# Performance work log

Measured on AMD Instinct MI355X. Metric: run time of the kernel, lower is better.

## Reference

```python
import jax, jax.numpy as jnp
import numpy as np

MAXLEN = 30
VOCAB_SIZE = 20000
THOUGHT = 1200
WORD = 620
BATCH = 130  # decoder uses B-2 = 128 sequences


def setup_inputs() -> dict:
    key = jax.random.key(0)
    ks = jax.random.split(key, 8)
    s_ih = 1.0 / np.sqrt(WORD)
    return {
        "thoughts": jax.random.normal(ks[0], (BATCH, THOUGHT), dtype=jnp.float32),
        "embed_table": jax.random.normal(ks[1], (VOCAB_SIZE, WORD), dtype=jnp.float32),
        "W_ih": jax.random.uniform(ks[2], (4 * WORD, 2 * THOUGHT + WORD), jnp.float32, -s_ih, s_ih),
        "W_hh": jax.random.uniform(ks[3], (4 * WORD, WORD), jnp.float32, -s_ih, s_ih),
        "b_ih": jax.random.uniform(ks[4], (4 * WORD,), jnp.float32, -s_ih, s_ih),
        "b_hh": jax.random.uniform(ks[5], (4 * WORD,), jnp.float32, -s_ih, s_ih),
        "Ww": jax.random.uniform(ks[6], (VOCAB_SIZE, WORD), jnp.float32, -s_ih, s_ih),
        "bw": jax.random.uniform(ks[7], (VOCAB_SIZE,), jnp.float32, -s_ih, s_ih),
    }


def reference(thoughts, embed_table, W_ih, W_hh, b_ih, b_hh, Ww, bw):
    # context: concat(thoughts_prev, thoughts_next) -> [B-2, 2*THOUGHT]
    ctx = jnp.concatenate([thoughts[:-2], thoughts[2:]], axis=1)
    n = ctx.shape[0]
    h0 = jnp.zeros((n, WORD), dtype=thoughts.dtype)  # (h,c) reset to 0 each step

    def step(last_word, _):
        x = jnp.concatenate([ctx, last_word], axis=1)  # [n, 3020]
        # LSTM cell with zero initial state (original discards state each step)
        gates = x @ W_ih.T + b_ih + h0 @ W_hh.T + b_hh  # [n, 4*WORD]
        i, f, g, o = jnp.split(gates, 4, axis=1)
        c = jax.nn.sigmoid(i) * jnp.tanh(g)  # f-gate irrelevant, c_prev = 0
        h = jax.nn.sigmoid(o) * jnp.tanh(c)  # [n, WORD]
        logits = h @ Ww.T + bw               # [n, VOCAB]
        idx = jnp.argmax(logits, axis=1)
        new_last = embed_table[idx]          # greedy-decoded word embedding
        return new_last, h

    _, hs = jax.lax.scan(step, h0, None, length=MAXLEN)  # [MAXLEN, n, WORD]
    pred = jnp.einsum("tnw,vw->tnv", hs, Ww) + bw        # [MAXLEN, n, VOCAB]
    return jnp.transpose(pred, (1, 0, 2))                 # [n, MAXLEN, VOCAB]
```

## Files before the change

### kernel.cpp

```cpp
#include <hip/hip_runtime.h>
#include <math.h>

#define VOCAB 20000
#define WORD 620
#define NSEQ 128
#define TMAX 30
#define CTXK 2400
#define XK 3020
#define NBLK 256

typedef unsigned long long u64;
typedef __attribute__((ext_vector_type(8))) short short8;
typedef __attribute__((ext_vector_type(4))) float f32x4;

__device__ __forceinline__ unsigned ford(float f) {
    unsigned b = __float_as_uint(f);
    return (b & 0x80000000u) ? ~b : (b | 0x80000000u);
}
__device__ __forceinline__ unsigned short bf16rne(float x) {
    unsigned u = __float_as_uint(x);
    return (unsigned short)((u + 0x7fffu + ((u >> 16) & 1u)) >> 16);
}
__device__ __forceinline__ float bf16tof(unsigned short h) {
    return __uint_as_float(((unsigned)h) << 16);
}
__device__ __forceinline__ short8 ld8(const unsigned short* p) {
    return *(const short8*)p;
}
#define MFMA(a, b, c) __builtin_amdgcn_mfma_f32_16x16x32_bf16((a), (b), (c), 0, 0, 0)
#define VMW(N) asm volatile("s_waitcnt vmcnt(" #N ")" ::: "memory")
#define AL64(p) __hip_atomic_load((p), __ATOMIC_RELAXED, __HIP_MEMORY_SCOPE_AGENT)

__device__ __forceinline__ void gload_lds16(const void* g, void* l) {
    __builtin_amdgcn_global_load_lds((const __attribute__((address_space(1))) void*)g,
                                     (__attribute__((address_space(3))) void*)l,
                                     16, 0, 0);
}

__device__ __forceinline__ void gridbar(unsigned* bar, unsigned epoch, bool rel) {
    __syncthreads();
    if (threadIdx.x == 0) {
        if (rel) __threadfence();
        unsigned g = blockIdx.x >> 4;
        unsigned a = __hip_atomic_fetch_add(&bar[g * 16], 1u, __ATOMIC_RELAXED, __HIP_MEMORY_SCOPE_AGENT);
        if (a == epoch * 16u - 1u)
            __hip_atomic_fetch_add(&bar[256], 1u, __ATOMIC_RELAXED, __HIP_MEMORY_SCOPE_AGENT);
        while (__hip_atomic_load(&bar[256], __ATOMIC_RELAXED, __HIP_MEMORY_SCOPE_AGENT) < epoch * 16u)
            __builtin_amdgcn_s_sleep(2);
    }
    __syncthreads();
}


__global__ __launch_bounds__(256) void kpack_w(const float* __restrict__ src,
                                               unsigned short* __restrict__ dst,
                                               int nvt, int nks, int col0,
                                               int ncols_valid, int src_ld,
                                               int nrows_valid, int rowmap) {
    int i = blockIdx.x * 256 + threadIdx.x;
    if (i >= nvt * nks * 512) return;
    int j = i & 7;
    int lane = (i >> 3) & 63;
    int t2 = i >> 9;
    int ks = t2 % nks;
    int vt = t2 / nks;
    int r = vt * 16 + (lane & 15);
    int k = ks * 32 + ((lane >> 4) << 3) + j;
    float x = 0.f;
    if (r < nrows_valid && k < ncols_valid) {
        int row = (rowmap == 1) ? ((r < 620) ? r : r + 620) : r;
        x = src[(size_t)row * src_ld + col0 + k];
    }
    unsigned short hi = bf16rne(x);
    unsigned short lo = bf16rne(x - bf16tof(hi));
    size_t ob = (size_t)t2 * 1024 + lane * 8 + j;
    dst[ob] = hi;
    dst[ob + 512] = lo;
}

__global__ __launch_bounds__(256) void kpack_ctx(const float* __restrict__ th,
                                                 unsigned short* __restrict__ dst) {
    int i = blockIdx.x * 256 + threadIdx.x;
    if (i >= 75 * 8 * 512) return;
    int j = i & 7;
    int lane = (i >> 3) & 63;
    int t2 = i >> 9;
    int mt = t2 & 7;
    int ks = t2 >> 3;
    int n = mt * 16 + (lane & 15);
    int k = ks * 32 + ((lane >> 4) << 3) + j;
    float x = (k < 1200) ? th[(size_t)n * 1200 + k]
                         : th[(size_t)(n + 2) * 1200 + (k - 1200)];
    unsigned short hi = bf16rne(x);
    unsigned short lo = bf16rne(x - bf16tof(hi));
    size_t ob = (size_t)t2 * 1024 + lane * 8 + j;
    dst[ob] = hi;
    dst[ob + 512] = lo;
}

__global__ __launch_bounds__(256) void kpack_embed(const float* __restrict__ embed,
                                                   unsigned short* __restrict__ ehi,
                                                   unsigned short* __restrict__ elo) {
    size_t i = (size_t)blockIdx.x * 256 + threadIdx.x;
    if (i >= (size_t)VOCAB * 640) return;
    int v = (int)(i / 640);
    int k = (int)(i % 640);
    float x = (k < WORD) ? embed[(size_t)v * WORD + k] : 0.f;
    unsigned short hi = bf16rne(x);
    ehi[i] = hi;
    elo[i] = bf16rne(x - bf16tof(hi));
}

__global__ __launch_bounds__(256) void ggemm(const unsigned short* __restrict__ Af,
                                             const unsigned short* __restrict__ Bf,
                                             const float* __restrict__ addRow,
                                             const float* __restrict__ addFull,
                                             float* __restrict__ outT,
                                             int nks, int nvt, int ldout) {
    int lane = threadIdx.x & 63, wv = threadIdx.x >> 6;
    int vtb = blockIdx.x * 8 + wv * 2;
    bool ok0 = vtb < nvt, ok1 = (vtb + 1) < nvt;
    f32x4 acc[8][2];
#pragma unroll
    for (int m = 0; m < 8; ++m) { acc[m][0] = (f32x4)0.f; acc[m][1] = (f32x4)0.f; }
    if (ok0) {
        const unsigned short* ap = Af + lane * 8;
        const unsigned short* bp0 = Bf + (size_t)vtb * nks * 1024 + lane * 8;
        const unsigned short* bp1 = bp0 + (size_t)nks * 1024;
        for (int ks = 0; ks < nks; ++ks) {
            short8 b0h = ld8(bp0), b0l = ld8(bp0 + 512);
            short8 ah[8], al[8];
#pragma unroll
            for (int m = 0; m < 8; ++m) {
                ah[m] = ld8(ap + m * 1024);
                al[m] = ld8(ap + m * 1024 + 512);
            }
#pragma unroll
            for (int m = 0; m < 8; ++m) {
                acc[m][0] = MFMA(ah[m], b0h, acc[m][0]);
                acc[m][0] = MFMA(ah[m], b0l, acc[m][0]);
                acc[m][0] = MFMA(al[m], b0h, acc[m][0]);
            }
            if (ok1) {
                short8 b1h = ld8(bp1), b1l = ld8(bp1 + 512);
#pragma unroll
                for (int m = 0; m < 8; ++m) {
                    acc[m][1] = MFMA(ah[m], b1h, acc[m][1]);
                    acc[m][1] = MFMA(ah[m], b1l, acc[m][1]);
                    acc[m][1] = MFMA(al[m], b1h, acc[m][1]);
                }
            }
            ap += 8192; bp0 += 1024; bp1 += 1024;
        }
    }
    int rbase = (lane >> 4) << 2;
    int cof = lane & 15;
#pragma unroll
    for (int v = 0; v < 2; ++v) {
        bool ok = v ? ok1 : ok0;
        if (!ok) continue;
        int col = (vtb + v) * 16 + cof;
        float ar = addRow ? addRow[col] : 0.f;
#pragma unroll
        for (int m = 0; m < 8; ++m) {
#pragma unroll
            for (int r = 0; r < 4; ++r) {
                int row = m * 16 + rbase + r;
                float x = acc[m][v][r] + ar;
                if (addFull) x += addFull[(size_t)row * ldout + col];
                outT[(size_t)row * ldout + col] = x;
            }
        }
    }
}

__global__ __launch_bounds__(256) void kinit3(unsigned* hf32, unsigned* slots32,
                                              float* bsum, unsigned* bar,
                                              const float* __restrict__ b_ih,
                                              const float* __restrict__ b_hh) {
    int i = blockIdx.x * 256 + threadIdx.x;
    if (i < 81920) hf32[i] = 0u;
    if (i < 7680) slots32[i] = 0u;
    if (i < 512) bar[i] = 0u;
    if (i < 1872) {
        float v = 0.f;
        if (i < 1860) {
            int row = (i < 620) ? i : i + 620;
            v = b_ih[row] + b_hh[row];
        }
        bsum[i] = v;
    }
}

__global__ __launch_bounds__(512, 2) void kmega(
    const unsigned short* __restrict__ embhi,
    const unsigned short* __restrict__ emblo,
    const unsigned short* __restrict__ Wgf3,
    const unsigned short* __restrict__ Wwf,
    const float* __restrict__ base,
    const float* __restrict__ bw,
    unsigned short* __restrict__ hf,
    u64* __restrict__ slots,
    float* __restrict__ out,
    unsigned* bar) {
    __shared__ char sBhi[102400];
    __shared__ char sA[3][16384];
    __shared__ u64 keybuf[128];
    const int tid = threadIdx.x;
    const int lane = tid & 63;
    const int wv = tid >> 6;
    const int bid = blockIdx.x;

    const int vt_lo = (int)(((long long)bid * 1250) / NBLK);
    const int vt_hi = (int)(((long long)(bid + 1) * 1250) / NBLK);
    const int nvt = vt_hi - vt_lo;
    const bool act = (wv < nvt);
    const int myvt = vt_lo + (act ? wv : 0);
    const bool gact = (bid < 39);

    const char* hfb = (const char*)hf;
    const char* wwb = (const char*)Wwf;
    const unsigned short* BbaseLo = Wwf + (size_t)myvt * 20480 + 512 + lane * 8;
    unsigned epoch = 0;

    for (int i = wv; i < nvt * 20; i += 8) {
        const char* g = wwb + (size_t)(vt_lo + i / 20) * 40960 + (size_t)(i % 20) * 2048 + lane * 16;
        gload_lds16(g, sBhi + (size_t)i * 1024);
    }
    VMW(0);
    __syncthreads();

    u64 R[3][4];
    short8 Bl[4];

#define ISSUE(M)                                                               \
    do {                                                                       \
        const u64* ga_ = (const u64*)(hfb + (size_t)(M) * 16384 +              \
                                      wv * 2048 + lane * 16);                  \
        R[(M) % 3][0] = AL64(ga_ + 0);                                         \
        R[(M) % 3][1] = AL64(ga_ + 1);                                         \
        R[(M) % 3][2] = AL64(ga_ + 128);                                       \
        R[(M) % 3][3] = AL64(ga_ + 129);                                       \
        if (act) Bl[(M) % 4] = ld8(BbaseLo + (size_t)(M) * 1024);              \
    } while (0)

#define WRA(M)                                                                 \
    do {                                                                       \
        u64* da_ = (u64*)(sA[(M) % 3] + wv * 2048 + lane * 16);                \
        da_[0] = R[(M) % 3][0];                                                \
        da_[1] = R[(M) % 3][1];                                                \
        da_[128] = R[(M) % 3][2];                                              \
        da_[129] = R[(M) % 3][3];                                              \
    } while (0)

#define LSTEP(K)                                                               \
    do {                                                                       \
        if ((K) + 3 < 20) ISSUE((K) + 3);                                      \
        if ((K) <= 16) { if (act) { VMW(10); } else { VMW(8); } }              \
        else if ((K) == 17) { if (act) { VMW(5); } else { VMW(4); } }          \
        else { VMW(0); }                                                       \
        if ((K) + 1 < 20) WRA((K) + 1);                                        \
        asm volatile("s_waitcnt lgkmcnt(0)" ::: "memory");                     \
        __builtin_amdgcn_s_barrier();                                          \
        __builtin_amdgcn_sched_barrier(0);                                     \
        if (act) {                                                             \
            const unsigned short* ab_ = (const unsigned short*)sA[(K) % 3];    \
            short8 bh_ = ld8((const unsigned short*)(sBhi +                    \
                             (size_t)(wv * 20 + (K)) * 1024) + lane * 8);      \
            _Pragma("unroll")                                                  \
            for (int mt = 0; mt < 8; ++mt) {                                   \
                short8 ah_ = ld8(ab_ + mt * 1024 + lane * 8);                  \
                short8 al_ = ld8(ab_ + mt * 1024 + 512 + lane * 8);            \
                acc[mt] = MFMA(ah_, bh_, acc[mt]);                             \
                acc[mt] = MFMA(ah_, Bl[(K) % 4], acc[mt]);                     \
                acc[mt] = MFMA(al_, bh_, acc[mt]);                             \
            }                                                                  \
        }                                                                      \
    } while (0)

    for (int t = 0; t < TMAX; ++t) {
        if (gact) {
            const int g_vt = bid;
            const int g_mt = wv;
            f32x4 aI = (f32x4)0.f, aG = (f32x4)0.f, aO = (f32x4)0.f;
            if (t > 0) {
                int n = g_mt * 16 + (lane & 15);
                u64 s = AL64(&slots[(size_t)(t - 1) * NSEQ + n]);
                unsigned idx = 0xFFFFFFFFu - (unsigned)(s & 0xFFFFFFFFull);
                const unsigned short* eh = embhi + (size_t)idx * 640 + ((lane >> 4) << 3);
                const unsigned short* el = emblo + (size_t)idx * 640 + ((lane >> 4) << 3);
                const unsigned short* bI = Wgf3 + (size_t)(0 * 39 + g_vt) * 20480 + lane * 8;
                const unsigned short* bG = Wgf3 + (size_t)(1 * 39 + g_vt) * 20480 + lane * 8;
                const unsigned short* bO = Wgf3 + (size_t)(2 * 39 + g_vt) * 20480 + lane * 8;
#pragma unroll 2
                for (int ks = 0; ks < 20; ++ks) {
                    short8 ah = ld8(eh + ks * 32);
                    short8 al = ld8(el + ks * 32);
                    short8 bIh = ld8(bI), bIl = ld8(bI + 512);
                    short8 bGh = ld8(bG), bGl = ld8(bG + 512);
                    short8 bOh = ld8(bO), bOl = ld8(bO + 512);
                    aI = MFMA(ah, bIh, aI); aI = MFMA(ah, bIl, aI); aI = MFMA(al, bIh, aI);
                    aG = MFMA(ah, bGh, aG); aG = MFMA(ah, bGl, aG); aG = MFMA(al, bGh, aG);
                    aO = MFMA(ah, bOh, aO); aO = MFMA(ah, bOl, aO); aO = MFMA(al, bOh, aO);
                    bI += 1024; bG += 1024; bO += 1024;
                }
            }
            int col = g_vt * 16 + (lane & 15);
            if (col < WORD) {
                int rbase = g_mt * 16 + ((lane >> 4) << 2);
#pragma unroll
                for (int r = 0; r < 4; ++r) {
                    int n = rbase + r;
                    float gi = aI[r] + base[(size_t)n * 1872 + col];
                    float gg = aG[r] + base[(size_t)n * 1872 + 620 + col];
                    float go = aO[r] + base[(size_t)n * 1872 + 1240 + col];
                    float si = 1.f / (1.f + expf(-gi));
                    float so = 1.f / (1.f + expf(-go));
                    float h = so * tanhf(si * tanhf(gg));
                    int pos = (((col >> 5) * 8 + (n >> 4)) * 1024) +
                              (((n & 15) + (((col & 31) >> 3) << 4)) * 8) + (col & 7);
                    unsigned short hi = bf16rne(h);
                    hf[pos] = hi;
                    hf[pos + 512] = bf16rne(h - bf16tof(hi));
                }
            }
        }
        if (tid < 128) keybuf[tid] = 0ull;
        ++epoch;
        gridbar(bar, epoch, gact);

        f32x4 acc[8];
#pragma unroll
        for (int mt = 0; mt < 8; ++mt) acc[mt] = (f32x4)0.f;

        ISSUE(0);
        ISSUE(1);
        ISSUE(2);
        if (act) { VMW(10); } else { VMW(8); }
        WRA(0);

        LSTEP(0);  LSTEP(1);  LSTEP(2);  LSTEP(3);  LSTEP(4);
        LSTEP(5);  LSTEP(6);  LSTEP(7);  LSTEP(8);  LSTEP(9);
        LSTEP(10); LSTEP(11); LSTEP(12); LSTEP(13); LSTEP(14);
        LSTEP(15); LSTEP(16); LSTEP(17); LSTEP(18); LSTEP(19);

        int q = lane >> 4, cof = lane & 15;
        if (act) {
            int v = myvt * 16 + cof;
            float bwv = bw[v];
#pragma unroll
            for (int mt = 0; mt < 8; ++mt) {
#pragma unroll
                for (int r = 0; r < 4; ++r) {
                    int n = mt * 16 + q * 4 + r;
                    float x = acc[mt][r] + bwv;
                    __builtin_nontemporal_store(x, &out[((size_t)n * TMAX + t) * VOCAB + v]);
                    u64 key = ((u64)ford(x) << 32) | (u64)(0xFFFFFFFFu - (unsigned)v);
#pragma unroll
                    for (int s2 = 1; s2 <= 8; s2 <<= 1) {
                        u64 o = __shfl_xor(key, s2, 64);
                        if (o > key) key = o;
                    }
                    if (cof == 0) atomicMax(&keybuf[n], key);
                }
            }
        }
        __syncthreads();
        if (tid < 128) {
            u64 k = keybuf[tid];
            if (k) atomicMax(&slots[(size_t)t * NSEQ + tid], k);
        }
        if (t + 1 < TMAX) {
            ++epoch;
            gridbar(bar, epoch, false);
        }
    }
#undef LSTEP
#undef WRA
#undef ISSUE
}

__global__ __launch_bounds__(256) void kinit2(unsigned int* lastfrag32,
                                              unsigned int* hfrag32,
                                              unsigned int* slots32,
                                              float* bsum,
                                              const float* __restrict__ b_ih,
                                              const float* __restrict__ b_hh) {
    int i = blockIdx.x * 256 + threadIdx.x;
    if (i < 81920) { lastfrag32[i] = 0u; hfrag32[i] = 0u; }
    if (i < 7680) slots32[i] = 0u;
    if (i < 1872) {
        float v = 0.f;
        if (i < 1860) {
            int row = (i < 620) ? i : i + 620;
            v = b_ih[row] + b_hh[row];
        }
        bsum[i] = v;
    }
}

__global__ __launch_bounds__(256) void klogits2(const unsigned short* __restrict__ Hf,
                                                const unsigned short* __restrict__ Wf,
                                                const float* __restrict__ bw,
                                                float* __restrict__ out,
                                                u64* __restrict__ slots, int t) {
    __shared__ u64 keybuf[128];
    int tid = threadIdx.x;
    if (tid < 128) keybuf[tid] = 0ull;
    __syncthreads();
    int lane = tid & 63, wv = tid >> 6;
    int vtb = blockIdx.x * 8 + wv * 2;
    bool ok0 = vtb < 1250, ok1 = (vtb + 1) < 1250;
    f32x4 acc[8][2];
#pragma unroll
    for (int m = 0; m < 8; ++m) { acc[m][0] = (f32x4)0.f; acc[m][1] = (f32x4)0.f; }
    if (ok0) {
        const unsigned short* ap = Hf + lane * 8;
        const unsigned short* bp0 = Wf + (size_t)vtb * 20 * 1024 + lane * 8;
        const unsigned short* bp1 = bp0 + 20 * 1024;
#pragma unroll 2
        for (int ks = 0; ks < 20; ++ks) {
            short8 b0h = ld8(bp0), b0l = ld8(bp0 + 512);
            short8 ah[8], al[8];
#pragma unroll
            for (int m = 0; m < 8; ++m) {
                ah[m] = ld8(ap + m * 1024);
                al[m] = ld8(ap + m * 1024 + 512);
            }
#pragma unroll
            for (int m = 0; m < 8; ++m) {
                acc[m][0] = MFMA(ah[m], b0h, acc[m][0]);
                acc[m][0] = MFMA(ah[m], b0l, acc[m][0]);
                acc[m][0] = MFMA(al[m], b0h, acc[m][0]);
            }
            if (ok1) {
                short8 b1h = ld8(bp1), b1l = ld8(bp1 + 512);
#pragma unroll
                for (int m = 0; m < 8; ++m) {
                    acc[m][1] = MFMA(ah[m], b1h, acc[m][1]);
                    acc[m][1] = MFMA(ah[m], b1l, acc[m][1]);
                    acc[m][1] = MFMA(al[m], b1h, acc[m][1]);
                }
            }
            ap += 8192; bp0 += 1024; bp1 += 1024;
        }
    }
    int rbase = (lane >> 4) << 2;
    int cof = lane & 15;
    float bw0 = ok0 ? bw[vtb * 16 + cof] : 0.f;
    float bw1 = ok1 ? bw[(vtb + 1) * 16 + cof] : 0.f;
#pragma unroll
    for (int m = 0; m < 8; ++m) {
#pragma unroll
        for (int r = 0; r < 4; ++r) {
            int row = m * 16 + rbase + r;
            u64 km = 0ull;
            if (ok0) {
                int v = vtb * 16 + cof;
                float x = acc[m][0][r] + bw0;
                out[((size_t)row * TMAX + t) * VOCAB + v] = x;
                km = ((u64)ford(x) << 32) | (u64)(0xFFFFFFFFu - (unsigned)v);
            }
            if (ok1) {
                int v = (vtb + 1) * 16 + cof;
                float x = acc[m][1][r] + bw1;
                out[((size_t)row * TMAX + t) * VOCAB + v] = x;
                u64 k2 = ((u64)ford(x) << 32) | (u64)(0xFFFFFFFFu - (unsigned)v);
                if (k2 > km) km = k2;
            }
#pragma unroll
            for (int s2 = 1; s2 <= 8; s2 <<= 1) {
                u64 o = __shfl_xor(km, s2, 64);
                if (o > km) km = o;
            }
            if ((lane & 15) == 0 && km) atomicMax(&keybuf[row], km);
        }
    }
    __syncthreads();
    if (tid < 128) atomicMax(&slots[(size_t)t * NSEQ + tid], keybuf[tid]);
}

__global__ void kact(const float* __restrict__ gates,
                     unsigned short* __restrict__ hfrag) {
    int n = blockIdx.x;
    int k = threadIdx.x;
    if (k >= WORD) return;
    const float* g = gates + (size_t)n * 1872;
    float gi = g[k], gg = g[620 + k], go = g[1240 + k];
    float si = 1.f / (1.f + expf(-gi));
    float so = 1.f / (1.f + expf(-go));
    float h = so * tanhf(si * tanhf(gg));
    int ks = k >> 5, mt = n >> 4;
    int lane = (n & 15) + (((k & 31) >> 3) << 4);
    int j = k & 7;
    size_t ob = (size_t)(ks * 8 + mt) * 1024 + lane * 8 + j;
    unsigned short hi = bf16rne(h);
    hfrag[ob] = hi;
    hfrag[ob + 512] = bf16rne(h - bf16tof(hi));
}

__global__ void kgather2(const float* __restrict__ embed,
                         const u64* __restrict__ slots,
                         unsigned short* __restrict__ lastfrag, int t) {
    int n = blockIdx.x;
    int k = threadIdx.x;
    if (k >= WORD) return;
    u64 s = slots[(size_t)t * NSEQ + n];
    unsigned idx = 0xFFFFFFFFu - (unsigned)(s & 0xFFFFFFFFull);
    float x = embed[(size_t)idx * WORD + k];
    int ks = k >> 5, mt = n >> 4;
    int lane = (n & 15) + (((k & 31) >> 3) << 4);
    int j = k & 7;
    size_t ob = (size_t)(ks * 8 + mt) * 1024 + lane * 8 + j;
    unsigned short hi = bf16rne(x);
    lastfrag[ob] = hi;
    lastfrag[ob + 512] = bf16rne(x - bf16tof(hi));
}

extern "C" void kernel_launch(void* const* d_in, const int* in_sizes, int n_in,
                              void* d_out, int out_size, void* d_ws, size_t ws_size,
                              hipStream_t stream) {
    const float* thoughts = (const float*)d_in[0];
    const float* embed    = (const float*)d_in[1];
    const float* W_ih     = (const float*)d_in[2];
    const float* b_ih     = (const float*)d_in[4];
    const float* b_hh     = (const float*)d_in[5];
    const float* Ww       = (const float*)d_in[6];
    const float* bw       = (const float*)d_in[7];
    float* out = (float*)d_out;
    char* ws = (char*)d_ws;

    const size_t OFF_WWF  = 0;
    const size_t OFF_WBF  = 51200000;
    const size_t OFF_WGF3 = 69171200;
    const size_t OFF_CTXF = 73963520;
    const size_t OFF_EHI  = 75192320;
    const size_t OFF_ELO  = 100792320;
    const size_t OFF_HF   = 126392320;
    const size_t OFF_BASE = 126720000;
    const size_t OFF_BSUM = 127678464;
    const size_t OFF_SLOT = 127685952;
    const size_t OFF_BAR  = 127716672;
    const size_t NEED_MEGA = 127718720;

    if (ws_size >= NEED_MEGA) {
        unsigned short* Wwf  = (unsigned short*)(ws + OFF_WWF);
        unsigned short* Wbf  = (unsigned short*)(ws + OFF_WBF);
        unsigned short* Wgf3 = (unsigned short*)(ws + OFF_WGF3);
        unsigned short* ctxf = (unsigned short*)(ws + OFF_CTXF);
        unsigned short* ehi  = (unsigned short*)(ws + OFF_EHI);
        unsigned short* elo  = (unsigned short*)(ws + OFF_ELO);
        unsigned short* hf   = (unsigned short*)(ws + OFF_HF);
        float* base = (float*)(ws + OFF_BASE);
        float* bsum = (float*)(ws + OFF_BSUM);
        u64*   slots = (u64*)(ws + OFF_SLOT);
        unsigned* bar = (unsigned*)(ws + OFF_BAR);

        kinit3<<<320, 256, 0, stream>>>((unsigned*)hf, (unsigned*)slots, bsum, bar, b_ih, b_hh);
        kpack_w<<<50000, 256, 0, stream>>>(Ww, Wwf, 1250, 20, 0, 620, WORD, VOCAB, 0);
        kpack_w<<<17550, 256, 0, stream>>>(W_ih, Wbf, 117, 75, 0, 2400, XK, 1860, 1);
        kpack_w<<<1560, 256, 0, stream>>>(W_ih + (size_t)0 * XK,    Wgf3 + 0 * 798720, 39, 20, 2400, 620, XK, 620, 0);
        kpack_w<<<1560, 256, 0, stream>>>(W_ih + (size_t)1240 * XK, Wgf3 + 1 * 798720, 39, 20, 2400, 620, XK, 620, 0);
        kpack_w<<<1560, 256, 0, stream>>>(W_ih + (size_t)1860 * XK, Wgf3 + 2 * 798720, 39, 20, 2400, 620, XK, 620, 0);
        kpack_ctx<<<1200, 256, 0, stream>>>(thoughts, ctxf);
        kpack_embed<<<50000, 256, 0, stream>>>(embed, ehi, elo);
        ggemm<<<15, 256, 0, stream>>>(ctxf, Wbf, bsum, nullptr, base, 75, 117, 1872);

        kmega<<<NBLK, 512, 0, stream>>>(ehi, elo, Wgf3, Wwf, base, bw, hf, slots, out, bar);
    } else {
        const size_t F_WWF  = 0;
        const size_t F_WBF  = 51200000;
        const size_t F_WGF  = 69171200;
        const size_t F_CTXF = 73963520;
        const size_t F_HF   = 75192320;
        const size_t F_LF   = 75520000;
        const size_t F_BASE = 75847680;
        const size_t F_GATE = 76806144;
        const size_t F_BSUM = 77764608;
        const size_t F_SLOT = 77772096;

        unsigned short* Wwf  = (unsigned short*)(ws + F_WWF);
        unsigned short* Wbf  = (unsigned short*)(ws + F_WBF);
        unsigned short* Wgf  = (unsigned short*)(ws + F_WGF);
        unsigned short* ctxf = (unsigned short*)(ws + F_CTXF);
        unsigned short* hf   = (unsigned short*)(ws + F_HF);
        unsigned short* lf   = (unsigned short*)(ws + F_LF);
        float* base = (float*)(ws + F_BASE);
        float* gate = (float*)(ws + F_GATE);
        float* bsum = (float*)(ws + F_BSUM);
        u64*   slots = (u64*)(ws + F_SLOT);

        kinit2<<<320, 256, 0, stream>>>((unsigned int*)lf, (unsigned int*)hf,
                                        (unsigned int*)slots, bsum, b_ih, b_hh);
        kpack_w<<<50000, 256, 0, stream>>>(Ww, Wwf, 1250, 20, 0, 620, WORD, VOCAB, 0);
        kpack_w<<<17550, 256, 0, stream>>>(W_ih, Wbf, 117, 75, 0, 2400, XK, 1860, 1);
        kpack_w<<<4680, 256, 0, stream>>>(W_ih, Wgf, 117, 20, 2400, 620, XK, 1860, 1);
        kpack_ctx<<<1200, 256, 0, stream>>>(thoughts, ctxf);
        ggemm<<<15, 256, 0, stream>>>(ctxf, Wbf, bsum, nullptr, base, 75, 117, 1872);
        for (int t = 0; t < TMAX; ++t) {
            ggemm<<<15, 256, 0, stream>>>(lf, Wgf, nullptr, base, gate, 20, 117, 1872);
            kact<<<NSEQ, 640, 0, stream>>>(gate, hf);
            klogits2<<<157, 256, 0, stream>>>(hf, Wwf, bw, out, slots, t);
            if (t + 1 < TMAX)
                kgather2<<<NSEQ, 640, 0, stream>>>(embed, slots, lf, t);
        }
    }
}
```

Baseline: 1.527 ms.

## Split grid barriers into targeted producer/consumer flags and defer logits stores

Replaces the two full-grid barriers per timestep with split arrive/wait counters. Only the 39 gate blocks wait for the argmax-completion counter, and all blocks wait on a separate counter covering just those 39 gate blocks before consuming h. The large nontemporal logits store is moved after the block signals its argmax arrival, so the output writes overlap with the next step's gate computation on other blocks. The risk is that ordering and memory visibility now rest on the new counter arithmetic and the bar[] slots it uses.

```diff
diff --git a/kernel.cpp b/kernel.cpp
--- a/kernel.cpp
+++ b/kernel.cpp
@@ -30,25 +30,13 @@
 #define MFMA(a, b, c) __builtin_amdgcn_mfma_f32_16x16x32_bf16((a), (b), (c), 0, 0, 0)
 #define VMW(N) asm volatile("s_waitcnt vmcnt(" #N ")" ::: "memory")
 #define AL64(p) __hip_atomic_load((p), __ATOMIC_RELAXED, __HIP_MEMORY_SCOPE_AGENT)
+#define AADD(p) __hip_atomic_fetch_add((p), 1u, __ATOMIC_RELAXED, __HIP_MEMORY_SCOPE_AGENT)
+#define ALD(p) __hip_atomic_load((p), __ATOMIC_RELAXED, __HIP_MEMORY_SCOPE_AGENT)
 
 __device__ __forceinline__ void gload_lds16(const void* g, void* l) {
     __builtin_amdgcn_global_load_lds((const __attribute__((address_space(1))) void*)g,
                                      (__attribute__((address_space(3))) void*)l,
                                      16, 0, 0);
-}
-
-__device__ __forceinline__ void gridbar(unsigned* bar, unsigned epoch, bool rel) {
-    __syncthreads();
-    if (threadIdx.x == 0) {
-        if (rel) __threadfence();
-        unsigned g = blockIdx.x >> 4;
-        unsigned a = __hip_atomic_fetch_add(&bar[g * 16], 1u, __ATOMIC_RELAXED, __HIP_MEMORY_SCOPE_AGENT);
-        if (a == epoch * 16u - 1u)
-            __hip_atomic_fetch_add(&bar[256], 1u, __ATOMIC_RELAXED, __HIP_MEMORY_SCOPE_AGENT);
-        while (__hip_atomic_load(&bar[256], __ATOMIC_RELAXED, __HIP_MEMORY_SCOPE_AGENT) < epoch * 16u)
-            __builtin_amdgcn_s_sleep(2);
-    }
-    __syncthreads();
 }
 
 
@@ -221,7 +209,6 @@
     const char* hfb = (const char*)hf;
     const char* wwb = (const char*)Wwf;
     const unsigned short* BbaseLo = Wwf + (size_t)myvt * 20480 + 512 + lane * 8;
-    unsigned epoch = 0;
 
     for (int i = wv; i < nvt * 20; i += 8) {
         const char* g = wwb + (size_t)(vt_lo + i / 20) * 40960 + (size_t)(i % 20) * 2048 + lane * 16;
@@ -280,6 +267,12 @@
 
     for (int t = 0; t < TMAX; ++t) {
         if (gact) {
+            if (t > 0) {
+                if (tid == 0)
+                    while (ALD(&bar[256]) < 16u * (unsigned)t)
+                        __builtin_amdgcn_s_sleep(2);
+                __syncthreads();
+            }
             const int g_vt = bid;
             const int g_mt = wv;
             f32x4 aI = (f32x4)0.f, aG = (f32x4)0.f, aO = (f32x4)0.f;
@@ -324,10 +317,22 @@
                     hf[pos + 512] = bf16rne(h - bf16tof(hi));
                 }
             }
-        }
+            __syncthreads();
+            if (tid == 0) {
+                __threadfence();
+                unsigned g = (unsigned)bid >> 3;
+                unsigned sz = (g < 4) ? 8u : 7u;
+                unsigned a = AADD(&bar[272 + g * 16]);
+                if (a == (unsigned)(t + 1) * sz - 1u)
+                    AADD(&bar[352]);
+            }
+        }
+
         if (tid < 128) keybuf[tid] = 0ull;
-        ++epoch;
-        gridbar(bar, epoch, gact);
+        if (tid == 0)
+            while (ALD(&bar[352]) < 5u * (unsigned)(t + 1))
+                __builtin_amdgcn_s_sleep(2);
+        __syncthreads();
 
         f32x4 acc[8];
 #pragma unroll
@@ -354,7 +359,6 @@
                 for (int r = 0; r < 4; ++r) {
                     int n = mt * 16 + q * 4 + r;
                     float x = acc[mt][r] + bwv;
-                    __builtin_nontemporal_store(x, &out[((size_t)n * TMAX + t) * VOCAB + v]);
                     u64 key = ((u64)ford(x) << 32) | (u64)(0xFFFFFFFFu - (unsigned)v);
 #pragma unroll
                     for (int s2 = 1; s2 <= 8; s2 <<= 1) {
@@ -370,9 +374,25 @@
             u64 k = keybuf[tid];
             if (k) atomicMax(&slots[(size_t)t * NSEQ + tid], k);
         }
-        if (t + 1 < TMAX) {
-            ++epoch;
-            gridbar(bar, epoch, false);
+        __syncthreads();
+        if (tid == 0) {
+            unsigned g = (unsigned)bid >> 4;
+            unsigned a = AADD(&bar[g * 16]);
+            if (a == (unsigned)(t + 1) * 16u - 1u)
+                AADD(&bar[256]);
+        }
+        if (act) {
+            int v = myvt * 16 + cof;
+            float bwv = bw[v];
+#pragma unroll
+            for (int mt = 0; mt < 8; ++mt) {
+#pragma unroll
+                for (int r = 0; r < 4; ++r) {
+                    int n = mt * 16 + q * 4 + r;
+                    float x = acc[mt][r] + bwv;
+                    __builtin_nontemporal_store(x, &out[((size_t)n * TMAX + t) * VOCAB + v]);
+                }
+            }
         }
     }
 #undef LSTEP
```

New measurement: 1.572 ms. 1.03x slower.
